# Kernel optimization log

Measured on AMD Instinct MI355X. Metric: run time of the kernel, lower is better.

The kernel has to match this reference:

```python
import jax, jax.numpy as jnp
import numpy as np

B, S, HN, TN = 8, 32, 64, 512
HID, EMB, VOCAB = 512, 512, 10000


def setup_inputs():
    key = jax.random.key(0)
    k = jax.random.split(key, 14)
    w = lambda kk, shape: jax.random.normal(kk, shape, jnp.float32) * 0.02
    return {
        "dec_out": jax.random.normal(k[0], (B, S, HID), jnp.float32),
        "history": jax.random.normal(k[1], (B, HID), jnp.float32),
        "head": jax.random.randint(k[2], (B, HN), 0, VOCAB),
        "tail": jax.random.randint(k[3], (B, TN), 0, VOCAB),
        "adj_mask": jax.random.randint(k[4], (B, HN, TN), 0, 2).astype(bool),
        "dup_mask": jax.random.randint(k[5], (B, S, TN), 0, 2).astype(bool),
        "emb_table": w(k[6], (VOCAB, EMB)),
        "W_tq": w(k[7], (2 * HID + EMB, HID)),
        "b_tq": jnp.zeros((HID,), jnp.float32),
        "W_tk": w(k[8], (EMB, HID)),
        "b_tk": jnp.zeros((HID,), jnp.float32),
        "W_tout": w(k[9], (2 * HID, HID)),
        "W_hq": w(k[10], (2 * HID, HID)),
        "b_hq": jnp.zeros((HID,), jnp.float32),
        "W_hk": w(k[11], (HID, HID)),
        "b_hk": jnp.zeros((HID,), jnp.float32),
    }


def reference(dec_out, history, head, tail, adj_mask, dup_mask, emb_table,
              W_tq, b_tq, W_tk, b_tk, W_tout, W_hq, b_hq, W_hk, b_hk):
    head_emb = emb_table[head]  # (B, HN, EMB)
    tail_emb = emb_table[tail]  # (B, TN, EMB)

    # --- tail attention query: Linear(cat([dec_out, history, head_emb])) + ELU.
    # Same math as the torch broadcast-concat, computed as a sum of three
    # partial matmuls to avoid materializing the (B,S,HN,2*hid+emb) concat.
    Wd, Wh, We = W_tq[:HID], W_tq[HID:2 * HID], W_tq[2 * HID:]
    tq = jax.nn.elu((dec_out @ Wd)[:, :, None, :]
                    + (history @ Wh)[:, None, None, :]
                    + (head_emb @ We)[:, None, :, :]
                    + b_tq)                       # (B, S, HN, HID)
    tq = tq.reshape(B, S * HN, HID)
    tk = jax.nn.elu(tail_emb @ W_tk + b_tk)       # (B, TN, HID)  (dropout=eval)

    # combined logical mask: allowed = adjacency AND not-duplicate
    mask = (adj_mask[:, None, :, :] & ~dup_mask[:, :, None, :]).reshape(B, S * HN, TN)

    # GlobalAttention (dot): score -> mask -> softmax -> context -> tanh(linear_out([c;q]))
    scores = jnp.einsum('bqh,bth->bqt', tq, tk)   # (B, S*HN, TN)
    tail_attn = jax.nn.softmax(jnp.where(mask, scores, -jnp.inf), axis=-1)
    ctx = jnp.einsum('bqt,bth->bqh', tail_attn, tk)
    graph_hid = jnp.tanh(ctx @ W_tout[:HID] + tq @ W_tout[HID:])
    graph_hid = graph_hid.reshape(B * S, HN, HID)
    tail_attn = tail_attn.reshape(B * S, HN, TN)

    # --- head attention (one-step), length-masked over HN
    hq = jax.nn.elu(dec_out @ W_hq[:HID] + (history @ W_hq[HID:])[:, None, :] + b_hq)
    hq = hq.reshape(B * S, HID)
    hk = jax.nn.elu(jnp.einsum('nkh,hd->nkd', graph_hid, W_hk) + b_hk)
    lengths = jnp.repeat(jnp.sum(head != 0, axis=-1), S)          # (B*S,)
    hscores = jnp.einsum('nh,nkh->nk', hq, hk)                    # (B*S, HN)
    lmask = jnp.arange(HN)[None, :] < lengths[:, None]
    head_attn = jax.nn.softmax(jnp.where(lmask, hscores, -jnp.inf), axis=-1)
    # (head-attention context output is discarded by the original module)

    prob = jnp.einsum('nk,nkt->nt', head_attn, tail_attn).reshape(B, S, TN)
    return jnp.log(prob + 1e-20)
```

## Files before the change

kernel.cpp:

```cpp
#include <hip/hip_runtime.h>
#include <math.h>

#define BB 8
#define SS 32
#define HN 64
#define TN 512
#define HID 512

typedef __attribute__((ext_vector_type(8))) short short8;
typedef __attribute__((ext_vector_type(4))) float f32x4;

__device__ __forceinline__ float eluf(float x) { return x > 0.f ? x : (expf(x) - 1.f); }

__device__ __forceinline__ short f2bs(float f) {
    union { float f; unsigned int u; } v; v.f = f;
    unsigned int r = v.u + 0x7fffu + ((v.u >> 16) & 1u);
    return (short)(r >> 16);
}
__device__ __forceinline__ float b2f(short s) {
    union { unsigned int u; float f; } v;
    v.u = ((unsigned int)(unsigned short)s) << 16;
    return v.f;
}

__device__ __forceinline__ void gld16(const void* g, void* l) {
    __builtin_amdgcn_global_load_lds(
        (const __attribute__((address_space(1))) void*)g,
        (__attribute__((address_space(3))) void*)l, 16, 0, 0);
}

template <int ACT, int OUTB>
__device__ __forceinline__ void gcore(
    const short* __restrict__ A, const short* __restrict__ B,
    const float* __restrict__ bias, void* __restrict__ Cv,
    int ldc, int K, int m0, int n0, int cm0, short* Ls)
{
    short* Al = Ls;
    short* Bl = Ls + 8192;
    const int tid  = threadIdx.x;
    const int lane = tid & 63;
    const int w    = tid >> 6;
    const int wr   = w >> 1, wc = w & 1;
    const int l16  = lane & 15, quad = lane >> 4;

    const int srow = w * 16 + (lane >> 2);
    const int scol = (lane & 3) * 8;

    f32x4 acc[4][4];
#pragma unroll
    for (int i = 0; i < 4; ++i)
#pragma unroll
        for (int j = 0; j < 4; ++j) { acc[i][j][0]=0.f; acc[i][j][1]=0.f; acc[i][j][2]=0.f; acc[i][j][3]=0.f; }

    short* lA = Al + w * 512;
    short* lB = Bl + w * 512;
    const long rstep = (long)64 * K;

    const short* Ag = A + (long)(m0 + srow) * K + scol;
    const short* Bg = B + (long)(n0 + srow) * K + scol;
    for (int kt = 0; kt < K; kt += 64) {
        __syncthreads();
        gld16(Ag + kt, lA);
        gld16(Ag + kt + rstep, lA + 2048);
        gld16(Ag + kt + 32, lA + 4096);
        gld16(Ag + kt + 32 + rstep, lA + 4096 + 2048);
        gld16(Bg + kt, lB);
        gld16(Bg + kt + rstep, lB + 2048);
        gld16(Bg + kt + 32, lB + 4096);
        gld16(Bg + kt + 32 + rstep, lB + 4096 + 2048);
        __syncthreads();
#pragma unroll
        for (int h = 0; h < 2; ++h) {
            short8 af[4], bf4[4];
#pragma unroll
            for (int mi = 0; mi < 4; ++mi)
                af[mi] = *(const short8*)(Al + h * 4096 + (wr * 64 + mi * 16 + l16) * 32 + quad * 8);
#pragma unroll
            for (int ni = 0; ni < 4; ++ni)
                bf4[ni] = *(const short8*)(Bl + h * 4096 + (wc * 64 + ni * 16 + l16) * 32 + quad * 8);
#pragma unroll
            for (int mi = 0; mi < 4; ++mi)
#pragma unroll
                for (int ni = 0; ni < 4; ++ni)
                    acc[mi][ni] = __builtin_amdgcn_mfma_f32_16x16x32_bf16(af[mi], bf4[ni], acc[mi][ni], 0, 0, 0);
        }
    }

    __syncthreads();

    float bv[4];
#pragma unroll
    for (int ni = 0; ni < 4; ++ni)
        bv[ni] = bias ? bias[n0 + wc * 64 + ni * 16 + l16] : 0.f;

    if (OUTB == 1) {
        short* eb = Ls + w * 1152;
        const int er = lane >> 2;
        const int ec = (lane & 3) * 16;
#pragma unroll
        for (int mi = 0; mi < 4; ++mi) {
#pragma unroll
            for (int ni = 0; ni < 4; ++ni)
#pragma unroll
                for (int r = 0; r < 4; ++r) {
                    float x = acc[mi][ni][r] + bv[ni];
                    if (ACT == 1) x = eluf(x);
                    eb[(quad * 4 + r) * 72 + ni * 16 + l16] = f2bs(x);
                }
            __builtin_amdgcn_sched_barrier(0);
            short8 v0 = *(const short8*)&eb[er * 72 + ec];
            short8 v1 = *(const short8*)&eb[er * 72 + ec + 8];
            long cb = (long)(cm0 + wr * 64 + mi * 16 + er) * ldc + n0 + wc * 64 + ec;
            *(short8*)((short*)Cv + cb)     = v0;
            *(short8*)((short*)Cv + cb + 8) = v1;
            __builtin_amdgcn_sched_barrier(0);
        }
    } else {
#pragma unroll
        for (int mi = 0; mi < 4; ++mi)
#pragma unroll
            for (int ni = 0; ni < 4; ++ni) {
                int gc = n0 + wc * 64 + ni * 16 + l16;
#pragma unroll
                for (int r = 0; r < 4; ++r) {
                    float x = acc[mi][ni][r] + bv[ni];
                    if (ACT == 1) x = eluf(x);
                    ((float*)Cv)[(long)(cm0 + wr * 64 + mi * 16 + quad * 4 + r) * ldc + gc] = x;
                }
            }
    }
}

#define L_TQ   0
#define L_BST  32768
#define L_AST  65536
#define L_EB   69632
#define L_HQ   78848
#define L_TOT  79872

template <int AFT>
__device__ __forceinline__ void tgemmv(
    const short* __restrict__ Arows, const short* __restrict__ B,
    short* Ls, f32x4 (&acc)[4][4])
{
    const int tid  = threadIdx.x;
    const int lane = tid & 63;
    const int w    = tid >> 6;
    const int l16  = lane & 15, quad = lane >> 4;
    short* TQ  = Ls + L_TQ;
    short* BST = Ls + L_BST;
    short* AST = Ls + L_AST;

    auto STAGE = [&](int kt, int p) {
        short* Bl = BST + p * 16384;
#pragma unroll
        for (int j = 0; j < 4; ++j) {
            int lin = j * 512 + tid;
            int r = lin >> 2, gs = lin & 3;
            int g = gs ^ ((r >> 1) & 3);
            gld16(B + (long)r * 512 + kt + g * 8, Bl + j * 4096 + w * 512);
        }
        if constexpr (AFT == 0) {
            if (tid < 256) {
                short* Al = AST + p * 2048;
                int r = tid >> 2, gs = tid & 3;
                int g = gs ^ ((r >> 1) & 3);
                gld16(Arows + (long)r * 512 + kt + g * 8, Al + w * 512);
            }
        }
    };

    STAGE(0, 0);
    int p = 0;
    for (int kt = 0; kt < 512; kt += 32, p ^= 1) {
        if (kt + 32 < 512) {
            STAGE(kt + 32, p ^ 1);
            if (AFT == 0 && w < 4) asm volatile("s_waitcnt vmcnt(5)" ::: "memory");
            else                   asm volatile("s_waitcnt vmcnt(4)" ::: "memory");
        } else {
            asm volatile("s_waitcnt vmcnt(0)" ::: "memory");
        }
        __builtin_amdgcn_s_barrier();
        __builtin_amdgcn_sched_barrier(0);

        short* Bl = BST + p * 16384;
        short8 af[4], bf[4];
#pragma unroll
        for (int mi = 0; mi < 4; ++mi) {
            int row = mi * 16 + l16;
            if constexpr (AFT == 1) {
                int slot = ((kt >> 3) + quad) ^ (row & 7);
                af[mi] = *(const short8*)(TQ + row * 512 + slot * 8);
            } else {
                short* Al = AST + p * 2048;
                int slot = quad ^ ((row >> 1) & 3);
                af[mi] = *(const short8*)(Al + row * 32 + slot * 8);
            }
        }
#pragma unroll
        for (int ni = 0; ni < 4; ++ni) {
            int row = w * 64 + ni * 16 + l16;
            int slot = quad ^ ((row >> 1) & 3);
            bf[ni] = *(const short8*)(Bl + row * 32 + slot * 8);
        }
        __builtin_amdgcn_s_setprio(1);
#pragma unroll
        for (int mi = 0; mi < 4; ++mi)
#pragma unroll
            for (int ni = 0; ni < 4; ++ni)
                acc[mi][ni] = __builtin_amdgcn_mfma_f32_16x16x32_bf16(af[mi], bf[ni], acc[mi][ni], 0, 0, 0);
        __builtin_amdgcn_s_setprio(0);
        asm volatile("s_waitcnt lgkmcnt(0)" ::: "memory");
        __builtin_amdgcn_s_barrier();
        __builtin_amdgcn_sched_barrier(0);
    }
}

template <int MODE>
__device__ __forceinline__ void epi(f32x4 (&acc)[4][4], short* Ls)
{
    const int tid  = threadIdx.x;
    const int lane = tid & 63;
    const int w    = tid >> 6;
    const int l16  = lane & 15, quad = lane >> 4;
    short* eb = Ls + L_EB + w * 1152;
    const int er = lane >> 2;
    const int ec = (lane & 3) * 16;
#pragma unroll
    for (int mi = 0; mi < 4; ++mi) {
#pragma unroll
        for (int ni = 0; ni < 4; ++ni)
#pragma unroll
            for (int r = 0; r < 4; ++r) {
                float x = acc[mi][ni][r];
                if (MODE == 1) x = tanhf(x);
                eb[(quad * 4 + r) * 72 + ni * 16 + l16] = f2bs(x);
            }
        __builtin_amdgcn_sched_barrier(0);
        short8 v0 = *(const short8*)&eb[er * 72 + ec];
        short8 v1 = *(const short8*)&eb[er * 72 + ec + 8];
        int row = mi * 16 + er;
        if (MODE == 0) {
            short* SC = Ls + L_BST;
            *(short8*)(SC + row * 512 + w * 64 + ec)     = v0;
            *(short8*)(SC + row * 512 + w * 64 + ec + 8) = v1;
        } else {
            int g0 = (w * 64 + ec) >> 3;
            *(short8*)(Ls + L_TQ + row * 512 + ((g0)     ^ (row & 7)) * 8) = v0;
            *(short8*)(Ls + L_TQ + row * 512 + ((g0 + 1) ^ (row & 7)) * 8) = v1;
        }
        __builtin_amdgcn_sched_barrier(0);
    }
}

__global__ __launch_bounds__(512, 1) void tail_kernel(
    const float* __restrict__ qall, const float* __restrict__ qe,
    const float* __restrict__ b_tq, const float* __restrict__ b_hq,
    const short* __restrict__ tkb, const short* __restrict__ tkWTb,
    const short* __restrict__ WT,
    const int* __restrict__ adj, const int* __restrict__ dup,
    const int* __restrict__ head, const float* __restrict__ b_hk,
    short* __restrict__ Pb, float* __restrict__ out)
{
    __shared__ short Ls[L_TOT];
    const int tid  = threadIdx.x;
    const int lane = tid & 63;
    const int w    = tid >> 6;
    const int l16  = lane & 15, quad = lane >> 4;

    const int n = (blockIdx.x & 7) * 32 + (blockIdx.x >> 3);
    const int b = n >> 5;
    const int s = n & 31;
    const long rb = (long)n * 64;

    const short* tkb_b  = tkb + (long)b * 262144;
    const short* tkWT_b = tkWTb + (long)b * 262144;
    const short* WT7    = WT + (size_t)7 * 262144;
    const short* WT8    = WT + (size_t)8 * 262144;
    short* Prows = Pb + rb * 512;
    float* HQ = (float*)(Ls + L_HQ);

    {
        const int cg = tid & 63;
        const int wg = tid >> 6;
        float4 qd0 = *(const float4*)(qall + (long)n * 2048 + cg * 8);
        float4 qd1 = *(const float4*)(qall + (long)n * 2048 + cg * 8 + 4);
        float4 qh0 = *(const float4*)(qall + (long)(256 + b) * 2048 + 1024 + cg * 8);
        float4 qh1 = *(const float4*)(qall + (long)(256 + b) * 2048 + 1024 + cg * 8 + 4);
        float4 bt0 = *(const float4*)(b_tq + cg * 8);
        float4 bt1 = *(const float4*)(b_tq + cg * 8 + 4);
        float base[8] = {qd0.x + qh0.x + bt0.x, qd0.y + qh0.y + bt0.y,
                         qd0.z + qh0.z + bt0.z, qd0.w + qh0.w + bt0.w,
                         qd1.x + qh1.x + bt1.x, qd1.y + qh1.y + bt1.y,
                         qd1.z + qh1.z + bt1.z, qd1.w + qh1.w + bt1.w};
#pragma unroll
        for (int i = 0; i < 8; ++i) {
            int h = wg * 8 + i;
            const float* er = qe + (long)(b * 64 + h) * 512 + cg * 8;
            float4 e0 = *(const float4*)er;
            float4 e1 = *(const float4*)(er + 4);
            float ev[8] = {e0.x, e0.y, e0.z, e0.w, e1.x, e1.y, e1.z, e1.w};
            short8 o;
#pragma unroll
            for (int u = 0; u < 8; ++u) o[u] = f2bs(eluf(base[u] + ev[u]));
            int slot = cg ^ (h & 7);
            *(short8*)(Ls + L_TQ + h * 512 + slot * 8) = o;
        }
        if (tid < 512) {
            HQ[tid] = eluf(qall[(long)n * 2048 + 512 + tid]
                         + qall[(long)(256 + b) * 2048 + 1536 + tid] + b_hq[tid]);
        }
    }
    __syncthreads();

    f32x4 acc[4][4];
#pragma unroll
    for (int i = 0; i < 4; ++i)
#pragma unroll
        for (int j = 0; j < 4; ++j) { acc[i][j][0]=0.f; acc[i][j][1]=0.f; acc[i][j][2]=0.f; acc[i][j][3]=0.f; }

    tgemmv<1>(nullptr, tkb_b, Ls, acc);
    epi<0>(acc, Ls);
    __syncthreads();

    {
        short* SC = Ls + L_BST;
        const int* dupr = dup + ((long)(b * 32 + s)) * 512 + lane * 8;
        int4 d0 = *(const int4*)dupr, d1 = *(const int4*)(dupr + 4);
        int dm[8] = {d0.x, d0.y, d0.z, d0.w, d1.x, d1.y, d1.z, d1.w};
        for (int j = 0; j < 8; ++j) {
            int row = w * 8 + j;
            short8 v8 = *(const short8*)(SC + row * 512 + lane * 8);
            const int* adjr = adj + ((long)(b * 64 + row)) * 512 + lane * 8;
            int4 a0 = *(const int4*)adjr, a1 = *(const int4*)(adjr + 4);
            int am[8] = {a0.x, a0.y, a0.z, a0.w, a1.x, a1.y, a1.z, a1.w};
            float v[8];
            float m = -INFINITY;
#pragma unroll
            for (int i = 0; i < 8; ++i) {
                v[i] = (am[i] && !dm[i]) ? b2f(v8[i]) : -INFINITY;
                m = fmaxf(m, v[i]);
            }
#pragma unroll
            for (int d = 32; d >= 1; d >>= 1) m = fmaxf(m, __shfl_xor(m, d));
            float sum = 0.f;
#pragma unroll
            for (int i = 0; i < 8; ++i) {
                float e = (m == -INFINITY) ? 0.f : expf(v[i] - m);
                v[i] = e; sum += e;
            }
#pragma unroll
            for (int d = 32; d >= 1; d >>= 1) sum += __shfl_xor(sum, d);
            float inv = sum > 0.f ? 1.f / sum : 0.f;
            short8 o;
#pragma unroll
            for (int i = 0; i < 8; ++i) o[i] = f2bs(v[i] * inv);
            *(short8*)(Prows + (long)row * 512 + lane * 8) = o;
        }
    }
    __syncthreads();

#pragma unroll
    for (int i = 0; i < 4; ++i)
#pragma unroll
        for (int j = 0; j < 4; ++j) { acc[i][j][0]=0.f; acc[i][j][1]=0.f; acc[i][j][2]=0.f; acc[i][j][3]=0.f; }
    tgemmv<1>(nullptr, WT7, Ls, acc);
    tgemmv<0>(Prows, tkWT_b, Ls, acc);
    epi<1>(acc, Ls);
    __syncthreads();

#pragma unroll
    for (int i = 0; i < 4; ++i)
#pragma unroll
        for (int j = 0; j < 4; ++j) { acc[i][j][0]=0.f; acc[i][j][1]=0.f; acc[i][j][2]=0.f; acc[i][j][3]=0.f; }
    tgemmv<1>(nullptr, WT8, Ls, acc);

    float* F     = (float*)(Ls + L_BST);
    float* redf  = F;
    float* hal   = F + 512;
    float* partf = F + 576;
    {
        float bv[4], hqv[4];
#pragma unroll
        for (int ni = 0; ni < 4; ++ni) {
            int col = w * 64 + ni * 16 + l16;
            bv[ni]  = b_hk[col];
            hqv[ni] = HQ[col];
        }
#pragma unroll
        for (int mi = 0; mi < 4; ++mi)
#pragma unroll
            for (int r = 0; r < 4; ++r) {
                float p = 0.f;
#pragma unroll
                for (int ni = 0; ni < 4; ++ni)
                    p += eluf(acc[mi][ni][r] + bv[ni]) * hqv[ni];
                p += __shfl_xor(p, 1);
                p += __shfl_xor(p, 2);
                p += __shfl_xor(p, 4);
                p += __shfl_xor(p, 8);
                if (l16 == 0) redf[w * 64 + mi * 16 + quad * 4 + r] = p;
            }
    }
    __syncthreads();

    if (tid < 64) {
        float sv_raw = 0.f;
#pragma unroll
        for (int w2 = 0; w2 < 8; ++w2) sv_raw += redf[w2 * 64 + tid];
        int hv = head[b * 64 + tid];
        unsigned long long ball = __ballot(hv != 0);
        int len = __popcll(ball);
        float sv = (tid < len) ? sv_raw : -INFINITY;
        float m = sv;
#pragma unroll
        for (int d = 32; d >= 1; d >>= 1) m = fmaxf(m, __shfl_xor(m, d));
        float e = expf(sv - m);
        float sum = e;
#pragma unroll
        for (int d = 32; d >= 1; d >>= 1) sum += __shfl_xor(sum, d);
        hal[tid] = e / sum;
    }
    __syncthreads();

    {
        const short* tab = Prows + (long)(w * 8) * 512 + lane * 8;
        float a2[8] = {};
#pragma unroll
        for (int k = 0; k < 8; ++k) {
            float a = hal[w * 8 + k];
            short8 tv = *(const short8*)(tab + (long)k * 512);
#pragma unroll
            for (int u = 0; u < 8; ++u) a2[u] += a * b2f(tv[u]);
        }
        float4* pp = (float4*)&partf[w * 512 + lane * 8];
        pp[0] = make_float4(a2[0], a2[1], a2[2], a2[3]);
        pp[1] = make_float4(a2[4], a2[5], a2[6], a2[7]);
    }
    __syncthreads();

    {
        float a = 0.f;
#pragma unroll
        for (int w2 = 0; w2 < 8; ++w2) a += partf[w2 * 512 + tid];
        out[(long)n * 512 + tid] = logf(a + 1e-20f);
    }
}

struct WTDesc { const float* src[9]; short* dst[9]; };

__global__ __launch_bounds__(256) void prep(
    const float* __restrict__ dec_out, const float* __restrict__ history,
    short* __restrict__ decb,
    const float* __restrict__ emb, const int* __restrict__ head, const int* __restrict__ tail,
    short* __restrict__ embAll, WTDesc wd)
{
    __shared__ float t[32][33];
    const int id = blockIdx.x, tid = threadIdx.x;
    if (id < 132) {
        int i = (id * 256 + tid) * 4;
        float4 v = (i < 131072) ? *(const float4*)(dec_out + i)
                                : *(const float4*)(history + (i - 131072));
        short4 o;
        o.x = f2bs(v.x); o.y = f2bs(v.y); o.z = f2bs(v.z); o.w = f2bs(v.w);
        *(short4*)(decb + i) = o;
    } else if (id < 132 + 2304) {
        int r = (id - 132) * 2 + (tid >> 7);
        int c4 = (tid & 127) * 4;
        int idx = (r < 512) ? head[r] : tail[r - 512];
        float4 v = *(const float4*)(emb + (long)idx * 512 + c4);
        short4 o;
        o.x = f2bs(v.x); o.y = f2bs(v.y); o.z = f2bs(v.z); o.w = f2bs(v.w);
        *(short4*)(embAll + (long)r * 512 + c4) = o;
    } else {
        int q = id - 2436;
        int z = q >> 8, xy = q & 255;
        int x = xy & 15, y = xy >> 4;
        const float* src = wd.src[z];
        short* dst = wd.dst[z];
        int k0 = y * 32, n0 = x * 32;
        int tx = tid & 31, ty = tid >> 5;
#pragma unroll
        for (int i = 0; i < 32; i += 8)
            t[ty + i][tx] = src[(long)(k0 + ty + i) * 512 + n0 + tx];
        __syncthreads();
#pragma unroll
        for (int i = 0; i < 32; i += 8)
            dst[(long)(n0 + ty + i) * 512 + k0 + tx] = f2bs(t[tx][ty + i]);
    }
}

__global__ __launch_bounds__(256) void mgemm_multi(
    const short* __restrict__ decb, const short* __restrict__ WTall, float* __restrict__ qall,
    const short* __restrict__ embAll, const short* __restrict__ WTe, float* __restrict__ qe,
    const short* __restrict__ WTk, const float* __restrict__ b_tk, short* __restrict__ tkb)
{
    __shared__ short Ls[16384];
    int id = blockIdx.x;
    if (id < 48) {
        int y = id >> 4, x = id & 15;
        gcore<0, 0>(decb, WTall, nullptr, qall, 2048, 512, y * 128, x * 128, y * 128, Ls);
    } else if (id < 64) {
        int id2 = id - 48, y = id2 >> 2, x = id2 & 3;
        gcore<0, 0>(embAll, WTe, nullptr, qe, 512, 512, y * 128, x * 128, y * 128, Ls);
    } else {
        int id3 = id - 64, y = id3 >> 2, x = id3 & 3;
        gcore<1, 1>(embAll, WTk, b_tk, tkb, 512, 512, 512 + y * 128, x * 128, y * 128, Ls);
    }
}

__global__ __launch_bounds__(256) void tkwt_kernel(
    const short* __restrict__ WTo1, const short* __restrict__ tkb, short* __restrict__ tkWTb)
{
    __shared__ short Ls[16384];
    int id = blockIdx.x;
    int z = id >> 4, r = id & 15;
    int x = r & 3, y = r >> 2;
    gcore<0, 1>(WTo1, tkb + (long)z * 262144, nullptr,
                tkWTb + (long)z * 262144, 512, 512, y * 128, x * 128, y * 128, Ls);
}

extern "C" void kernel_launch(void* const* d_in, const int* in_sizes, int n_in,
                              void* d_out, int out_size, void* d_ws, size_t ws_size,
                              hipStream_t stream)
{
    const float* dec_out = (const float*)d_in[0];
    const float* history = (const float*)d_in[1];
    const int*   head    = (const int*)d_in[2];
    const int*   tail    = (const int*)d_in[3];
    const int*   adj     = (const int*)d_in[4];
    const int*   dup     = (const int*)d_in[5];
    const float* emb     = (const float*)d_in[6];
    const float* W_tq    = (const float*)d_in[7];
    const float* b_tq    = (const float*)d_in[8];
    const float* W_tk    = (const float*)d_in[9];
    const float* b_tk    = (const float*)d_in[10];
    const float* W_tout  = (const float*)d_in[11];
    const float* W_hq    = (const float*)d_in[12];
    const float* b_hq    = (const float*)d_in[13];
    const float* W_hk    = (const float*)d_in[14];
    const float* b_hk    = (const float*)d_in[15];
    float* out = (float*)d_out;

    char* ws = (char*)d_ws;
    auto alloc = [&](size_t bytes) -> void* {
        char* p = ws;
        ws += (bytes + 255) & ~(size_t)255;
        return (void*)p;
    };
    short* decb   = (short*)alloc((size_t)384 * 512 * 2);
    short* embAll = (short*)alloc((size_t)4608 * 512 * 2);
    short* WT     = (short*)alloc((size_t)9 * 512 * 512 * 2);
    float* qall   = (float*)alloc((size_t)384 * 2048 * 4);
    float* qe     = (float*)alloc((size_t)512 * 512 * 4);
    short* tkb    = (short*)alloc((size_t)4096 * 512 * 2);
    short* tkWTb  = (short*)alloc((size_t)4096 * 512 * 2);
    short* Pb     = (short*)alloc((size_t)16384 * 512 * 2);

    WTDesc wd;
    wd.src[0] = W_tq;               wd.dst[0] = WT;
    wd.src[1] = W_hq;               wd.dst[1] = WT + (size_t)1 * 262144;
    wd.src[2] = W_tq + 512 * 512;   wd.dst[2] = WT + (size_t)2 * 262144;
    wd.src[3] = W_hq + 512 * 512;   wd.dst[3] = WT + (size_t)3 * 262144;
    wd.src[4] = W_tq + 1024 * 512;  wd.dst[4] = WT + (size_t)4 * 262144;
    wd.src[5] = W_tk;               wd.dst[5] = WT + (size_t)5 * 262144;
    wd.src[6] = W_tout;             wd.dst[6] = WT + (size_t)6 * 262144;
    wd.src[7] = W_tout + 512 * 512; wd.dst[7] = WT + (size_t)7 * 262144;
    wd.src[8] = W_hk;               wd.dst[8] = WT + (size_t)8 * 262144;

    prep<<<4740, 256, 0, stream>>>(dec_out, history, decb, emb, head, tail, embAll, wd);
    mgemm_multi<<<192, 256, 0, stream>>>(decb, WT, qall, embAll, WT + (size_t)4 * 262144, qe,
                                         WT + (size_t)5 * 262144, b_tk, tkb);
    tkwt_kernel<<<128, 256, 0, stream>>>(WT + (size_t)6 * 262144, tkb, tkWTb);
    tail_kernel<<<256, 512, 0, stream>>>(qall, qe, b_tq, b_hq, tkb, tkWTb, WT,
                                         adj, dup, head, b_hk, Pb, out);
}
```

Before: 202.3 us.

## Fuse tail-key projection GEMM into mgemm kernel with per-batch atomic flags

Merges the separate tkwt_kernel launch into mgemm_multi by appending 128 blocks that spin-wait on per-batch atomic counters. The producer blocks signal completion of each batch's tk tile with release increments. The consumer blocks then compute the W_tout·tk product as soon as their batch is ready. This removes one kernel launch and the full-grid barrier between the two GEMM stages, but it relies on the producer blocks being scheduled before or alongside the spinning consumers. It also adds a memset and a bounded spin loop.

```diff
diff --git a/kernel.cpp b/kernel.cpp
--- a/kernel.cpp
+++ b/kernel.cpp
@@ -493,7 +493,8 @@
 __global__ __launch_bounds__(256) void mgemm_multi(
     const short* __restrict__ decb, const short* __restrict__ WTall, float* __restrict__ qall,
     const short* __restrict__ embAll, const short* __restrict__ WTe, float* __restrict__ qe,
-    const short* __restrict__ WTk, const float* __restrict__ b_tk, short* __restrict__ tkb)
+    const short* __restrict__ WTk, const float* __restrict__ b_tk, short* __restrict__ tkb,
+    const short* __restrict__ WTo1, short* __restrict__ tkWTb, unsigned* __restrict__ flags)
 {
     __shared__ short Ls[16384];
     int id = blockIdx.x;
@@ -503,21 +504,31 @@
     } else if (id < 64) {
         int id2 = id - 48, y = id2 >> 2, x = id2 & 3;
         gcore<0, 0>(embAll, WTe, nullptr, qe, 512, 512, y * 128, x * 128, y * 128, Ls);
-    } else {
+    } else if (id < 192) {
         int id3 = id - 64, y = id3 >> 2, x = id3 & 3;
         gcore<1, 1>(embAll, WTk, b_tk, tkb, 512, 512, 512 + y * 128, x * 128, y * 128, Ls);
-    }
-}
-
-__global__ __launch_bounds__(256) void tkwt_kernel(
-    const short* __restrict__ WTo1, const short* __restrict__ tkb, short* __restrict__ tkWTb)
-{
-    __shared__ short Ls[16384];
-    int id = blockIdx.x;
-    int z = id >> 4, r = id & 15;
-    int x = r & 3, y = r >> 2;
-    gcore<0, 1>(WTo1, tkb + (long)z * 262144, nullptr,
-                tkWTb + (long)z * 262144, 512, 512, y * 128, x * 128, y * 128, Ls);
+        __syncthreads();
+        if (threadIdx.x == 0)
+            __hip_atomic_fetch_add(&flags[(y >> 2) * 16], 1u,
+                                   __ATOMIC_RELEASE, __HIP_MEMORY_SCOPE_AGENT);
+    } else {
+        int id4 = id - 192;
+        int z = id4 >> 4, r = id4 & 15;
+        int x = r & 3, y2 = r >> 2;
+        if (threadIdx.x == 0) {
+            int guard = 0;
+            while (__hip_atomic_load(&flags[z * 16], __ATOMIC_RELAXED,
+                                     __HIP_MEMORY_SCOPE_AGENT) < 16u) {
+                __builtin_amdgcn_s_sleep(8);
+                if (++guard > (1 << 22)) break;
+            }
+            (void)__hip_atomic_load(&flags[z * 16], __ATOMIC_ACQUIRE,
+                                    __HIP_MEMORY_SCOPE_AGENT);
+        }
+        __syncthreads();
+        gcore<0, 1>(WTo1, tkb + (long)z * 262144, nullptr,
+                    tkWTb + (long)z * 262144, 512, 512, y2 * 128, x * 128, y2 * 128, Ls);
+    }
 }
 
 extern "C" void kernel_launch(void* const* d_in, const int* in_sizes, int n_in,
@@ -548,6 +559,7 @@
         ws += (bytes + 255) & ~(size_t)255;
         return (void*)p;
     };
+    unsigned* flags = (unsigned*)alloc(512);
     short* decb   = (short*)alloc((size_t)384 * 512 * 2);
     short* embAll = (short*)alloc((size_t)4608 * 512 * 2);
     short* WT     = (short*)alloc((size_t)9 * 512 * 512 * 2);
@@ -568,10 +580,11 @@
     wd.src[7] = W_tout + 512 * 512; wd.dst[7] = WT + (size_t)7 * 262144;
     wd.src[8] = W_hk;               wd.dst[8] = WT + (size_t)8 * 262144;
 
+    hipMemsetAsync(flags, 0, 512, stream);
     prep<<<4740, 256, 0, stream>>>(dec_out, history, decb, emb, head, tail, embAll, wd);
-    mgemm_multi<<<192, 256, 0, stream>>>(decb, WT, qall, embAll, WT + (size_t)4 * 262144, qe,
-                                         WT + (size_t)5 * 262144, b_tk, tkb);
-    tkwt_kernel<<<128, 256, 0, stream>>>(WT + (size_t)6 * 262144, tkb, tkWTb);
+    mgemm_multi<<<320, 256, 0, stream>>>(decb, WT, qall, embAll, WT + (size_t)4 * 262144, qe,
+                                         WT + (size_t)5 * 262144, b_tk, tkb,
+                                         WT + (size_t)6 * 262144, tkWTb, flags);
     tail_kernel<<<256, 512, 0, stream>>>(qall, qe, b_tq, b_hq, tkb, tkWTb, WT,
                                          adj, dup, head, b_hk, Pb, out);
 }
```

Result: no change. 205.8 us (+1.7%).
